# Kernel tuning notes

Hardware: AMD Instinct MI355X
Metric: run time of the kernel (lower is better)

## Reference

```python
import jax, jax.numpy as jnp
import numpy as np

N = 50000
E = 600000
IN_DIM, FEAT_DIM, HID_DIM, OUT_DIM = 256, 128, 128, 64


def _glorot(key, shape):
    fan_in, fan_out = shape[0], shape[1]
    lim = jnp.sqrt(6.0 / (fan_in + fan_out))
    return jax.random.uniform(key, shape, jnp.float32, -lim, lim)


def setup_inputs() -> dict:
    key = jax.random.key(0)
    ks = jax.random.split(key, 10)
    x = jax.random.normal(ks[0], (N, IN_DIM), jnp.float32)
    edge_index = jax.random.randint(ks[1], (2, E), 0, N, jnp.int64)
    return {
        "x": x,
        "edge_index": edge_index,
        # linear_pre: input_dim -> feature_dim
        "W_pre": _glorot(ks[2], (IN_DIM, FEAT_DIM)),
        "b_pre": jnp.zeros((FEAT_DIM,), jnp.float32),
        # conv_first (SAGEConv feature_dim -> hidden_dim): lin_l (neighbors, bias), lin_r (root, no bias)
        "Wl1": _glorot(ks[3], (FEAT_DIM, HID_DIM)),
        "bl1": jnp.zeros((HID_DIM,), jnp.float32),
        "Wr1": _glorot(ks[4], (FEAT_DIM, HID_DIM)),
        # conv_out (SAGEConv hidden_dim -> output_dim)
        "Wl2": _glorot(ks[5], (HID_DIM, OUT_DIM)),
        "bl2": jnp.zeros((OUT_DIM,), jnp.float32),
        "Wr2": _glorot(ks[6], (HID_DIM, OUT_DIM)),
    }


def _sage_conv(x, src, dst, deg_inv, Wl, bl, Wr):
    # mean aggregation of source features at destination nodes
    msgs = x[src]                                            # [E, d]
    aggr = jax.ops.segment_sum(msgs, dst, num_segments=N)    # [N, d]
    aggr = aggr * deg_inv[:, None]
    return aggr @ Wl + bl + x @ Wr


def reference(x, edge_index, W_pre, b_pre, Wl1, bl1, Wr1, Wl2, bl2, Wr2):
    src, dst = edge_index[0], edge_index[1]
    deg = jax.ops.segment_sum(jnp.ones((E,), jnp.float32), dst, num_segments=N)
    deg_inv = jnp.where(deg > 0, 1.0 / jnp.maximum(deg, 1.0), 0.0)

    h = x @ W_pre + b_pre                                    # linear_pre
    h = _sage_conv(h, src, dst, deg_inv, Wl1, bl1, Wr1)      # conv_first
    h = jax.nn.relu(h)
    # dropout: identity in eval mode
    h = _sage_conv(h, src, dst, deg_inv, Wl2, bl2, Wr2)      # conv_out
    norm = jnp.linalg.norm(h, axis=-1, keepdims=True)
    return h / jnp.maximum(norm, 1e-12)                      # F.normalize p=2
```

## Files before the change

kernel.cpp:

```cpp
#include <hip/hip_runtime.h>


#define NN   50000
#define EE   600000
#define NBLK 49
#define NRG64 782

typedef __attribute__((ext_vector_type(8))) _Float16 h8v;
typedef __attribute__((ext_vector_type(4))) _Float16 h4v;
typedef __attribute__((ext_vector_type(2))) _Float16 h2v;
typedef __attribute__((ext_vector_type(8))) short short8v;
typedef __attribute__((ext_vector_type(4))) float f32x4;

__device__ inline h8v h8zero() {
    return __builtin_bit_cast(h8v, (short8v){0,0,0,0,0,0,0,0});
}


__global__ __launch_bounds__(256) void k_count(const int* __restrict__ ei,
                                               int* __restrict__ counts) {
    int e = blockIdx.x * 256 + threadIdx.x;
    if (e < EE) atomicAdd(&counts[ei[EE + e]], 1);
}

__global__ __launch_bounds__(256) void k_scan_a(const int* __restrict__ counts,
                                                int* __restrict__ bsums) {
    int b = blockIdx.x, t = threadIdx.x;
    int idx = b * 1024 + t * 4;
    int s = 0;
#pragma unroll
    for (int j = 0; j < 4; ++j)
        if (idx + j < NN) s += counts[idx + j];
#pragma unroll
    for (int off = 32; off > 0; off >>= 1) s += __shfl_down(s, off);
    __shared__ int ls[4];
    if ((t & 63) == 0) ls[t >> 6] = s;
    __syncthreads();
    if (t == 0) bsums[b] = ls[0] + ls[1] + ls[2] + ls[3];
}

__global__ void k_scan_b(int* __restrict__ bsums) {
    int t = threadIdx.x;
    int v = (t < NBLK) ? bsums[t] : 0;
    int orig = v;
#pragma unroll
    for (int off = 1; off < 64; off <<= 1) {
        int u = __shfl_up(v, off);
        if (t >= off) v += u;
    }
    if (t < NBLK) bsums[t] = v - orig;
}

__global__ __launch_bounds__(256) void k_scan_c(const int* __restrict__ counts,
                                                const int* __restrict__ bsums,
                                                int* __restrict__ rowp) {
    int b = blockIdx.x, t = threadIdx.x;
    int lane = t & 63, wave = t >> 6;
    int idx = b * 1024 + t * 4;
    int c[4], s = 0;
#pragma unroll
    for (int j = 0; j < 4; ++j) {
        c[j] = (idx + j < NN) ? counts[idx + j] : 0;
        s += c[j];
    }
    int sv = s;
#pragma unroll
    for (int off = 1; off < 64; off <<= 1) {
        int u = __shfl_up(sv, off);
        if (lane >= off) sv += u;
    }
    __shared__ int lsum[4];
    if (lane == 63) lsum[wave] = sv;
    __syncthreads();
    int woff = 0;
    for (int wv = 0; wv < wave; ++wv) woff += lsum[wv];
    int base = bsums[b] + woff + (sv - s);
#pragma unroll
    for (int j = 0; j < 4; ++j) {
        if (idx + j < NN) { rowp[idx + j] = base; base += c[j]; }
    }
}

__global__ __launch_bounds__(256) void k_scatter(const int* __restrict__ ei,
                                                 const int* __restrict__ rowp,
                                                 int* __restrict__ cursor,
                                                 int* __restrict__ col) {
    int e = blockIdx.x * 256 + threadIdx.x;
    if (e < EE) {
        int d = ei[EE + e];
        int p = atomicAdd(&cursor[d], 1);
        col[rowp[d] + p] = ei[e];
    }
}


__global__ __launch_bounds__(256) void k_cvt(const float* __restrict__ in,
                                             _Float16* __restrict__ outp, int n4) {
    int i = blockIdx.x * 256 + threadIdx.x;
    if (i >= n4) return;
    float4 v = ((const float4*)in)[i];
    h4v o;
    o[0] = (_Float16)v.x; o[1] = (_Float16)v.y;
    o[2] = (_Float16)v.z; o[3] = (_Float16)v.w;
    ((h4v*)outp)[i] = o;
}


__global__ __launch_bounds__(256) void k_prep(const float* __restrict__ Wpre,
                                              const float* __restrict__ bpre,
                                              const float* __restrict__ Wl1,
                                              const float* __restrict__ Wr1,
                                              const float* __restrict__ Wl2,
                                              const float* __restrict__ Wr2,
                                              _Float16* __restrict__ WAH,
                                              _Float16* __restrict__ WAL,
                                              _Float16* __restrict__ WBH,
                                              _Float16* __restrict__ WBL,
                                              float* __restrict__ bA,
                                              float* __restrict__ bB,
                                              _Float16* __restrict__ W2lH,
                                              _Float16* __restrict__ W2lL,
                                              _Float16* __restrict__ W2rH,
                                              _Float16* __restrict__ W2rL) {
    int idx = blockIdx.x * 256 + threadIdx.x;
    if (idx < 65792) {
        int which = idx / (257 * 128);
        int rem = idx - which * 257 * 128;
        int i = rem >> 7, j = rem & 127;
        const float* W = which ? Wr1 : Wl1;
        float s = 0.f;
        if (i < 256) {
#pragma unroll 4
            for (int k = 0; k < 128; ++k) s += Wpre[i * 128 + k] * W[k * 128 + j];
            _Float16 h = (_Float16)s;
            _Float16 l = (_Float16)(s - (float)h);
            if (which) { WBH[j * 256 + i] = h; WBL[j * 256 + i] = l; }
            else       { WAH[j * 256 + i] = h; WAL[j * 256 + i] = l; }
        } else {
#pragma unroll 4
            for (int k = 0; k < 128; ++k) s += bpre[k] * W[k * 128 + j];
            if (which) bB[j] = s; else bA[j] = s;
        }
    } else {
        int idx2 = idx - 65792;
        int which = idx2 >> 13;
        int rem = idx2 & 8191;
        int k = rem >> 6, m = rem & 63;
        float w = (which ? Wr2 : Wl2)[rem];
        _Float16 h = (_Float16)w;
        _Float16 l = (_Float16)(w - (float)h);
        if (which) { W2rH[m * 128 + k] = h; W2rL[m * 128 + k] = l; }
        else       { W2lH[m * 128 + k] = h; W2lL[m * 128 + k] = l; }
    }
}


__global__ __launch_bounds__(256) void k_gemm_fused(
        const _Float16* __restrict__ xh,
        const _Float16* __restrict__ WAH, const _Float16* __restrict__ WAL,
        const _Float16* __restrict__ WBH, const _Float16* __restrict__ WBL,
        const float* __restrict__ bA, const float* __restrict__ bB,
        _Float16* __restrict__ t1, _Float16* __restrict__ r1) {
    __shared__ char As[64 * 512];
    const int t = threadIdx.x;
    const int wave = t >> 6, lane = t & 63;
    const int r = lane & 15, kb = lane >> 4;
    const int row0 = blockIdx.x << 6;

#pragma unroll
    for (int j = 0; j < 8; ++j) {
        int id = t + (j << 8);
        int row = id >> 5, c16 = id & 31;
        int gr = row0 + row;
        h8v v = (gr < NN) ? *(const h8v*)&xh[(size_t)gr * 256 + (c16 << 3)]
                          : h8zero();
        *(h8v*)&As[row * 512 + (((c16 << 4)) ^ ((row & 7) << 4))] = v;
    }
    __syncthreads();

    const int sel = wave >> 1;
    const _Float16* __restrict__ WH = sel ? WBH : WAH;
    const _Float16* __restrict__ WL = sel ? WBL : WAL;
    _Float16* __restrict__ dst = sel ? r1 : t1;
    const float* __restrict__ bias = sel ? bB : bA;
    const int colbase = (wave & 1) << 6;

    f32x4 acc[4][4];
#pragma unroll
    for (int sl = 0; sl < 4; ++sl)
#pragma unroll
        for (int rt = 0; rt < 4; ++rt) acc[sl][rt] = (f32x4){0.f, 0.f, 0.f, 0.f};

#pragma unroll
    for (int k = 0; k < 8; ++k) {
        h8v a[4];
#pragma unroll
        for (int rt = 0; rt < 4; ++rt) {
            int row = (rt << 4) + r;
            a[rt] = *(const h8v*)&As[row * 512 +
                                     (((k << 6) + (kb << 4)) ^ ((row & 7) << 4))];
        }
#pragma unroll
        for (int sl = 0; sl < 4; ++sl) {
            size_t woff = (size_t)(colbase + (sl << 4) + r) * 256 + (k << 5) + (kb << 3);
            h8v wh = *(const h8v*)&WH[woff];
            h8v wl = *(const h8v*)&WL[woff];
#pragma unroll
            for (int rt = 0; rt < 4; ++rt) {
                acc[sl][rt] = __builtin_amdgcn_mfma_f32_16x16x32_f16(a[rt], wh, acc[sl][rt], 0, 0, 0);
                acc[sl][rt] = __builtin_amdgcn_mfma_f32_16x16x32_f16(a[rt], wl, acc[sl][rt], 0, 0, 0);
            }
        }
    }
#pragma unroll
    for (int sl = 0; sl < 4; ++sl) {
        int col = colbase + (sl << 4) + r;
        float b = bias[col];
#pragma unroll
        for (int rt = 0; rt < 4; ++rt) {
            int rbase = row0 + (rt << 4) + (kb << 2);
#pragma unroll
            for (int j = 0; j < 4; ++j) {
                int rr = rbase + j;
                if (rr < NN)
                    dst[(size_t)rr * 128 + col] = (_Float16)(acc[sl][rt][j] + b);
            }
        }
    }
}


__global__ __launch_bounds__(256) void k_gemm_dual2(
        const _Float16* __restrict__ A,
        const _Float16* __restrict__ W1H, const _Float16* __restrict__ W1L,
        const _Float16* __restrict__ W2H, const _Float16* __restrict__ W2L,
        _Float16* __restrict__ T, _Float16* __restrict__ R) {
    __shared__ char As[64 * 256];
    const int t = threadIdx.x;
    const int wave = t >> 6, lane = t & 63;
    const int r = lane & 15, kb = lane >> 4;
    const int row0 = blockIdx.x << 6;

#pragma unroll
    for (int j = 0; j < 4; ++j) {
        int id = t + (j << 8);
        int row = id >> 4, c16 = id & 15;
        int gr = row0 + row;
        h8v v = (gr < NN) ? *(const h8v*)&A[(size_t)gr * 128 + (c16 << 3)]
                          : h8zero();
        *(h8v*)&As[row * 256 + (((c16 << 4)) ^ ((row & 7) << 4))] = v;
    }
    __syncthreads();

    const int sel = wave >> 1;
    const _Float16* __restrict__ WH = sel ? W2H : W1H;
    const _Float16* __restrict__ WL = sel ? W2L : W1L;
    _Float16* __restrict__ dst = sel ? R : T;
    const int colbase = (wave & 1) << 5;

    f32x4 acc[2][4];
#pragma unroll
    for (int sl = 0; sl < 2; ++sl)
#pragma unroll
        for (int rt = 0; rt < 4; ++rt) acc[sl][rt] = (f32x4){0.f, 0.f, 0.f, 0.f};

#pragma unroll
    for (int k = 0; k < 4; ++k) {
        h8v a[4];
#pragma unroll
        for (int rt = 0; rt < 4; ++rt) {
            int row = (rt << 4) + r;
            a[rt] = *(const h8v*)&As[row * 256 +
                                     (((k << 6) + (kb << 4)) ^ ((row & 7) << 4))];
        }
#pragma unroll
        for (int sl = 0; sl < 2; ++sl) {
            size_t woff = (size_t)(colbase + (sl << 4) + r) * 128 + (k << 5) + (kb << 3);
            h8v wh = *(const h8v*)&WH[woff];
            h8v wl = *(const h8v*)&WL[woff];
#pragma unroll
            for (int rt = 0; rt < 4; ++rt) {
                acc[sl][rt] = __builtin_amdgcn_mfma_f32_16x16x32_f16(a[rt], wh, acc[sl][rt], 0, 0, 0);
                acc[sl][rt] = __builtin_amdgcn_mfma_f32_16x16x32_f16(a[rt], wl, acc[sl][rt], 0, 0, 0);
            }
        }
    }
#pragma unroll
    for (int sl = 0; sl < 2; ++sl) {
        int col = colbase + (sl << 4) + r;
#pragma unroll
        for (int rt = 0; rt < 4; ++rt) {
            int rbase = row0 + (rt << 4) + (kb << 2);
#pragma unroll
            for (int j = 0; j < 4; ++j) {
                int rr = rbase + j;
                if (rr < NN)
                    dst[(size_t)rr * 64 + col] = (_Float16)acc[sl][rt][j];
            }
        }
    }
}


__global__ __launch_bounds__(256) void k_aggr1(const _Float16* __restrict__ t1,
                                               const _Float16* __restrict__ r1,
                                               const int* __restrict__ rowp,
                                               const int* __restrict__ counts,
                                               const int* __restrict__ col,
                                               const float* __restrict__ bl1,
                                               _Float16* __restrict__ h1) {
    int node = blockIdx.x * 4 + (threadIdx.x >> 6);
    int lane = threadIdx.x & 63;
    if (node >= NN) return;
    int half = lane >> 5, sl = lane & 31;
    int e0 = rowp[node], cnt = counts[node];
    float a0 = 0.f, a1 = 0.f, a2 = 0.f, a3 = 0.f;
    const h4v* T = (const h4v*)t1;
    for (int base = 0; base < cnt; base += 64) {
        int m = cnt - base; if (m > 64) m = 64;
        int myS = (base + lane < cnt) ? col[e0 + base + lane] : 0;
        int i = 0;
        for (; i + 8 <= m; i += 8) {
            int s0 = __shfl(myS, i + 0 + half), s1 = __shfl(myS, i + 2 + half);
            int s2 = __shfl(myS, i + 4 + half), s3 = __shfl(myS, i + 6 + half);
            h4v v0 = T[(size_t)s0 * 32 + sl], v1 = T[(size_t)s1 * 32 + sl];
            h4v v2 = T[(size_t)s2 * 32 + sl], v3 = T[(size_t)s3 * 32 + sl];
            a0 += (float)v0[0] + (float)v1[0] + (float)v2[0] + (float)v3[0];
            a1 += (float)v0[1] + (float)v1[1] + (float)v2[1] + (float)v3[1];
            a2 += (float)v0[2] + (float)v1[2] + (float)v2[2] + (float)v3[2];
            a3 += (float)v0[3] + (float)v1[3] + (float)v2[3] + (float)v3[3];
        }
        for (; i < m; i += 2) {
            if (i + half < m) {
                int s = __shfl(myS, i + half);
                h4v v = T[(size_t)s * 32 + sl];
                a0 += (float)v[0]; a1 += (float)v[1];
                a2 += (float)v[2]; a3 += (float)v[3];
            }
        }
    }
    a0 += __shfl_xor(a0, 32); a1 += __shfl_xor(a1, 32);
    a2 += __shfl_xor(a2, 32); a3 += __shfl_xor(a3, 32);
    float di = (cnt > 0) ? 1.0f / (float)cnt : 0.0f;
    h4v rr = ((const h4v*)r1)[(size_t)node * 32 + sl];
    float4 bb = ((const float4*)bl1)[sl];
    if (half == 0) {
        h4v h;
        h[0] = (_Float16)fmaxf(fmaf(a0, di, bb.x + (float)rr[0]), 0.0f);
        h[1] = (_Float16)fmaxf(fmaf(a1, di, bb.y + (float)rr[1]), 0.0f);
        h[2] = (_Float16)fmaxf(fmaf(a2, di, bb.z + (float)rr[2]), 0.0f);
        h[3] = (_Float16)fmaxf(fmaf(a3, di, bb.w + (float)rr[3]), 0.0f);
        ((h4v*)h1)[(size_t)node * 32 + sl] = h;
    }
}


__global__ __launch_bounds__(256) void k_aggr2(const _Float16* __restrict__ t2,
                                               const _Float16* __restrict__ r2,
                                               const int* __restrict__ rowp,
                                               const int* __restrict__ counts,
                                               const int* __restrict__ col,
                                               const float* __restrict__ bl2,
                                               float* __restrict__ out) {
    int node = blockIdx.x * 4 + (threadIdx.x >> 6);
    int lane = threadIdx.x & 63;
    if (node >= NN) return;
    int half = lane >> 5, sl = lane & 31;
    int e0 = rowp[node], cnt = counts[node];
    float ax = 0.f, ay = 0.f;
    const h2v* T = (const h2v*)t2;
    for (int base = 0; base < cnt; base += 64) {
        int m = cnt - base; if (m > 64) m = 64;
        int myS = (base + lane < cnt) ? col[e0 + base + lane] : 0;
        int i = 0;
        for (; i + 8 <= m; i += 8) {
            int s0 = __shfl(myS, i + 0 + half), s1 = __shfl(myS, i + 2 + half);
            int s2 = __shfl(myS, i + 4 + half), s3 = __shfl(myS, i + 6 + half);
            h2v v0 = T[(size_t)s0 * 32 + sl], v1 = T[(size_t)s1 * 32 + sl];
            h2v v2 = T[(size_t)s2 * 32 + sl], v3 = T[(size_t)s3 * 32 + sl];
            ax += (float)v0[0] + (float)v1[0] + (float)v2[0] + (float)v3[0];
            ay += (float)v0[1] + (float)v1[1] + (float)v2[1] + (float)v3[1];
        }
        for (; i < m; i += 2) {
            if (i + half < m) {
                int s = __shfl(myS, i + half);
                h2v v = T[(size_t)s * 32 + sl];
                ax += (float)v[0]; ay += (float)v[1];
            }
        }
    }
    ax += __shfl_xor(ax, 32);
    ay += __shfl_xor(ay, 32);
    float di = (cnt > 0) ? 1.0f / (float)cnt : 0.0f;
    h2v rr = ((const h2v*)r2)[(size_t)node * 32 + sl];
    float2 bb = ((const float2*)bl2)[sl];
    float v0 = fmaf(ax, di, bb.x + (float)rr[0]);
    float v1 = fmaf(ay, di, bb.y + (float)rr[1]);
    float ss = v0 * v0 + v1 * v1;
#pragma unroll
    for (int off = 16; off > 0; off >>= 1) ss += __shfl_xor(ss, off);
    float inv = 1.0f / fmaxf(sqrtf(ss), 1e-12f);
    if (half == 0)
        ((float2*)out)[(size_t)node * 32 + sl] = make_float2(v0 * inv, v1 * inv);
}


extern "C" void kernel_launch(void* const* d_in, const int* in_sizes, int n_in,
                              void* d_out, int out_size, void* d_ws, size_t ws_size,
                              hipStream_t stream) {
    const float* x    = (const float*)d_in[0];
    const int*   ei   = (const int*)d_in[1];
    const float* Wpre = (const float*)d_in[2];
    const float* bpre = (const float*)d_in[3];
    const float* Wl1  = (const float*)d_in[4];
    const float* bl1  = (const float*)d_in[5];
    const float* Wr1  = (const float*)d_in[6];
    const float* Wl2  = (const float*)d_in[7];
    const float* bl2  = (const float*)d_in[8];
    const float* Wr2  = (const float*)d_in[9];
    float* out = (float*)d_out;

    char* w = (char*)d_ws;
    int* counts = (int*)w;  w += (size_t)NN * 4;
    int* cursor = (int*)w;  w += (size_t)NN * 4;
    int* rowp   = (int*)w;  w += (size_t)NN * 4;
    int* bsums  = (int*)w;  w += 256;
    int* col    = (int*)w;  w += (size_t)EE * 4;
    _Float16* WAH  = (_Float16*)w; w += (size_t)256 * 128 * 2;
    _Float16* WAL  = (_Float16*)w; w += (size_t)256 * 128 * 2;
    _Float16* WBH  = (_Float16*)w; w += (size_t)256 * 128 * 2;
    _Float16* WBL  = (_Float16*)w; w += (size_t)256 * 128 * 2;
    float*    bA   = (float*)w;    w += 128 * 4;
    float*    bB   = (float*)w;    w += 128 * 4;
    _Float16* W2lH = (_Float16*)w; w += (size_t)128 * 64 * 2;
    _Float16* W2lL = (_Float16*)w; w += (size_t)128 * 64 * 2;
    _Float16* W2rH = (_Float16*)w; w += (size_t)128 * 64 * 2;
    _Float16* W2rL = (_Float16*)w; w += (size_t)128 * 64 * 2;
    _Float16* xh   = (_Float16*)w; w += (size_t)NN * 256 * 2;
    _Float16* t1   = (_Float16*)w; w += (size_t)NN * 128 * 2;
    _Float16* r1   = (_Float16*)w; w += (size_t)NN * 128 * 2;
    _Float16* h1   = (_Float16*)w; w += (size_t)NN * 128 * 2;
    _Float16* t2   = (_Float16*)w; w += (size_t)NN * 64 * 2;
    _Float16* r2   = (_Float16*)w; w += (size_t)NN * 64 * 2;

    hipMemsetAsync(counts, 0, (size_t)NN * 8, stream);

    dim3 b256(256);
    dim3 gE((EE + 255) / 256);
    k_count<<<gE, b256, 0, stream>>>(ei, counts);
    k_scan_a<<<dim3(NBLK), b256, 0, stream>>>(counts, bsums);
    k_scan_b<<<dim3(1), dim3(64), 0, stream>>>(bsums);
    k_scan_c<<<dim3(NBLK), b256, 0, stream>>>(counts, bsums, rowp);
    k_scatter<<<gE, b256, 0, stream>>>(ei, rowp, cursor, col);

    k_cvt<<<dim3(NN * 256 / 4 / 256), b256, 0, stream>>>(x, xh, NN * 256 / 4);
    k_prep<<<dim3(321), b256, 0, stream>>>(Wpre, bpre, Wl1, Wr1, Wl2, Wr2,
                                           WAH, WAL, WBH, WBL, bA, bB,
                                           W2lH, W2lL, W2rH, W2rL);

    k_gemm_fused<<<dim3(NRG64), b256, 0, stream>>>(xh, WAH, WAL, WBH, WBL,
                                                   bA, bB, t1, r1);
    k_aggr1<<<dim3((NN + 3) / 4), b256, 0, stream>>>(t1, r1, rowp, counts, col, bl1, h1);
    k_gemm_dual2<<<dim3(NRG64), b256, 0, stream>>>(h1, W2lH, W2lL, W2rH, W2rL, t2, r2);
    k_aggr2<<<dim3((NN + 3) / 4), b256, 0, stream>>>(t2, r2, rowp, counts, col, bl2, out);
}
```

Before: 312.3 us.

## Fuse fp32-to-fp16 input conversion into first GEMM and vectorize output stores

Removes the separate conversion kernel and the fp16 copy of x: the fused GEMM now loads fp32 rows of x directly and converts them while staging into shared memory. This saves one full write and read of a 25 MB half-precision buffer plus a kernel launch. Both GEMMs also swap the MFMA operand order so each lane holds four consecutive output columns, which allows packed 8-byte half4 stores in place of scalar 2-byte stores. The cost is that the GEMM reads twice as many bytes of x per tile.

```diff
diff --git a/kernel.cpp b/kernel.cpp
--- a/kernel.cpp
+++ b/kernel.cpp
@@ -14,6 +14,15 @@
 
 __device__ inline h8v h8zero() {
     return __builtin_bit_cast(h8v, (short8v){0,0,0,0,0,0,0,0});
+}
+
+__device__ inline h8v cvt8f(float4 f0, float4 f1) {
+    h8v a;
+    a[0] = (_Float16)f0.x; a[1] = (_Float16)f0.y;
+    a[2] = (_Float16)f0.z; a[3] = (_Float16)f0.w;
+    a[4] = (_Float16)f1.x; a[5] = (_Float16)f1.y;
+    a[6] = (_Float16)f1.z; a[7] = (_Float16)f1.w;
+    return a;
 }
 
 
@@ -91,18 +100,6 @@
         int p = atomicAdd(&cursor[d], 1);
         col[rowp[d] + p] = ei[e];
     }
-}
-
-
-__global__ __launch_bounds__(256) void k_cvt(const float* __restrict__ in,
-                                             _Float16* __restrict__ outp, int n4) {
-    int i = blockIdx.x * 256 + threadIdx.x;
-    if (i >= n4) return;
-    float4 v = ((const float4*)in)[i];
-    h4v o;
-    o[0] = (_Float16)v.x; o[1] = (_Float16)v.y;
-    o[2] = (_Float16)v.z; o[3] = (_Float16)v.w;
-    ((h4v*)outp)[i] = o;
 }
 
 
@@ -156,7 +153,7 @@
 
 
 __global__ __launch_bounds__(256) void k_gemm_fused(
-        const _Float16* __restrict__ xh,
+        const float* __restrict__ x,
         const _Float16* __restrict__ WAH, const _Float16* __restrict__ WAL,
         const _Float16* __restrict__ WBH, const _Float16* __restrict__ WBL,
         const float* __restrict__ bA, const float* __restrict__ bB,
@@ -172,8 +169,14 @@
         int id = t + (j << 8);
         int row = id >> 5, c16 = id & 31;
         int gr = row0 + row;
-        h8v v = (gr < NN) ? *(const h8v*)&xh[(size_t)gr * 256 + (c16 << 3)]
-                          : h8zero();
+        h8v v;
+        if (gr < NN) {
+            float4 f0 = *(const float4*)&x[(size_t)gr * 256 + (c16 << 3)];
+            float4 f1 = *(const float4*)&x[(size_t)gr * 256 + (c16 << 3) + 4];
+            v = cvt8f(f0, f1);
+        } else {
+            v = h8zero();
+        }
         *(h8v*)&As[row * 512 + (((c16 << 4)) ^ ((row & 7) << 4))] = v;
     }
     __syncthreads();
@@ -207,23 +210,25 @@
             h8v wl = *(const h8v*)&WL[woff];
 #pragma unroll
             for (int rt = 0; rt < 4; ++rt) {
-                acc[sl][rt] = __builtin_amdgcn_mfma_f32_16x16x32_f16(a[rt], wh, acc[sl][rt], 0, 0, 0);
-                acc[sl][rt] = __builtin_amdgcn_mfma_f32_16x16x32_f16(a[rt], wl, acc[sl][rt], 0, 0, 0);
+                acc[sl][rt] = __builtin_amdgcn_mfma_f32_16x16x32_f16(wh, a[rt], acc[sl][rt], 0, 0, 0);
+                acc[sl][rt] = __builtin_amdgcn_mfma_f32_16x16x32_f16(wl, a[rt], acc[sl][rt], 0, 0, 0);
             }
         }
     }
 #pragma unroll
     for (int sl = 0; sl < 4; ++sl) {
-        int col = colbase + (sl << 4) + r;
-        float b = bias[col];
+        int col4 = colbase + (sl << 4) + (kb << 2);
+        float4 b4 = *(const float4*)&bias[col4];
 #pragma unroll
         for (int rt = 0; rt < 4; ++rt) {
-            int rbase = row0 + (rt << 4) + (kb << 2);
-#pragma unroll
-            for (int j = 0; j < 4; ++j) {
-                int rr = rbase + j;
-                if (rr < NN)
-                    dst[(size_t)rr * 128 + col] = (_Float16)(acc[sl][rt][j] + b);
+            int row = row0 + (rt << 4) + r;
+            if (row < NN) {
+                h4v o;
+                o[0] = (_Float16)(acc[sl][rt][0] + b4.x);
+                o[1] = (_Float16)(acc[sl][rt][1] + b4.y);
+                o[2] = (_Float16)(acc[sl][rt][2] + b4.z);
+                o[3] = (_Float16)(acc[sl][rt][3] + b4.w);
+                *(h4v*)&dst[(size_t)row * 128 + col4] = o;
             }
         }
     }
@@ -280,22 +285,24 @@
             h8v wl = *(const h8v*)&WL[woff];
 #pragma unroll
             for (int rt = 0; rt < 4; ++rt) {
-                acc[sl][rt] = __builtin_amdgcn_mfma_f32_16x16x32_f16(a[rt], wh, acc[sl][rt], 0, 0, 0);
-                acc[sl][rt] = __builtin_amdgcn_mfma_f32_16x16x32_f16(a[rt], wl, acc[sl][rt], 0, 0, 0);
+                acc[sl][rt] = __builtin_amdgcn_mfma_f32_16x16x32_f16(wh, a[rt], acc[sl][rt], 0, 0, 0);
+                acc[sl][rt] = __builtin_amdgcn_mfma_f32_16x16x32_f16(wl, a[rt], acc[sl][rt], 0, 0, 0);
             }
         }
     }
 #pragma unroll
     for (int sl = 0; sl < 2; ++sl) {
-        int col = colbase + (sl << 4) + r;
+        int col4 = colbase + (sl << 4) + (kb << 2);
 #pragma unroll
         for (int rt = 0; rt < 4; ++rt) {
-            int rbase = row0 + (rt << 4) + (kb << 2);
-#pragma unroll
-            for (int j = 0; j < 4; ++j) {
-                int rr = rbase + j;
-                if (rr < NN)
-                    dst[(size_t)rr * 64 + col] = (_Float16)acc[sl][rt][j];
+            int row = row0 + (rt << 4) + r;
+            if (row < NN) {
+                h4v o;
+                o[0] = (_Float16)acc[sl][rt][0];
+                o[1] = (_Float16)acc[sl][rt][1];
+                o[2] = (_Float16)acc[sl][rt][2];
+                o[3] = (_Float16)acc[sl][rt][3];
+                *(h4v*)&dst[(size_t)row * 64 + col4] = o;
             }
         }
     }
@@ -436,7 +443,6 @@
     _Float16* W2lL = (_Float16*)w; w += (size_t)128 * 64 * 2;
     _Float16* W2rH = (_Float16*)w; w += (size_t)128 * 64 * 2;
     _Float16* W2rL = (_Float16*)w; w += (size_t)128 * 64 * 2;
-    _Float16* xh   = (_Float16*)w; w += (size_t)NN * 256 * 2;
     _Float16* t1   = (_Float16*)w; w += (size_t)NN * 128 * 2;
     _Float16* r1   = (_Float16*)w; w += (size_t)NN * 128 * 2;
     _Float16* h1   = (_Float16*)w; w += (size_t)NN * 128 * 2;
@@ -453,12 +459,11 @@
     k_scan_c<<<dim3(NBLK), b256, 0, stream>>>(counts, bsums, rowp);
     k_scatter<<<gE, b256, 0, stream>>>(ei, rowp, cursor, col);
 
-    k_cvt<<<dim3(NN * 256 / 4 / 256), b256, 0, stream>>>(x, xh, NN * 256 / 4);
     k_prep<<<dim3(321), b256, 0, stream>>>(Wpre, bpre, Wl1, Wr1, Wl2, Wr2,
                                            WAH, WAL, WBH, WBL, bA, bB,
                                            W2lH, W2lL, W2rH, W2rL);
 
-    k_gemm_fused<<<dim3(NRG64), b256, 0, stream>>>(xh, WAH, WAL, WBH, WBL,
+    k_gemm_fused<<<dim3(NRG64), b256, 0, stream>>>(x, WAH, WAL, WBH, WBL,
                                                    bA, bB, t1, r1);
     k_aggr1<<<dim3((NN + 3) / 4), b256, 0, stream>>>(t1, r1, rowp, counts, col, bl1, h1);
     k_gemm_dual2<<<dim3(NRG64), b256, 0, stream>>>(h1, W2lH, W2lL, W2rH, W2rL, t2, r2);
```

Measured after the change: 293.6 us. 1.06x faster.
